# Kernel tuning notes

Measured on AMD Instinct MI355X. Metric: run time of the kernel, lower is better.

## Reference

```python
import jax, jax.numpy as jnp
import numpy as np
from jax import lax

B, T, D, H = 2, 2048, 512, 8
HD = D // H
EPS = 1e-5


def _layernorm(x, g, b):
    m = jnp.mean(x, axis=-1, keepdims=True)
    v = jnp.var(x, axis=-1, keepdims=True)
    return (x - m) / jnp.sqrt(v + EPS) * g + b


def setup_inputs() -> dict:
    key = jax.random.key(0)
    ks = jax.random.split(key, 16)
    s = 0.02
    return {
        "x": jax.random.normal(ks[0], (B, T, D), jnp.float32),
        "pe": jax.random.normal(ks[1], (B, T, D), jnp.float32),
        "conv_w": jax.random.normal(ks[2], (D, D, 3), jnp.float32) * s,   # OIH
        "conv_b": jnp.zeros((D,), jnp.float32),
        "in_proj_w": jax.random.normal(ks[3], (3 * D, D), jnp.float32) * s,
        "in_proj_b": jnp.zeros((3 * D,), jnp.float32),
        "out_proj_w": jax.random.normal(ks[4], (D, D), jnp.float32) * s,
        "out_proj_b": jnp.zeros((D,), jnp.float32),
        "ln1_g": jnp.ones((D,), jnp.float32),
        "ln1_b": jnp.zeros((D,), jnp.float32),
        "w1": jax.random.normal(ks[5], (2 * D, D), jnp.float32) * s,
        "b1": jnp.zeros((2 * D,), jnp.float32),
        "w2": jax.random.normal(ks[6], (D, 2 * D), jnp.float32) * s,
        "b2": jnp.zeros((D,), jnp.float32),
        "ln2_g": jnp.ones((D,), jnp.float32),
        "ln2_b": jnp.zeros((D,), jnp.float32),
    }


def reference(x, pe, conv_w, conv_b, in_proj_w, in_proj_b, out_proj_w,
              out_proj_b, ln1_g, ln1_b, w1, b1, w2, b2, ln2_g, ln2_b):
    Bv, Tv, Dv = x.shape
    window = max(Tv // 4, 1)
    half = window // 2
    idx = jnp.arange(Tv)
    blocked = jnp.abs(idx[:, None] - idx[None, :]) > half  # [T, T]
    mask = jnp.where(blocked, -jnp.inf, 0.0).astype(x.dtype)

    # Conv1d on values: x [B,T,D] -> [B,D,T], kernel3 pad1, back to [B,T,D]
    xT = jnp.transpose(x, (0, 2, 1))
    v_in = lax.conv_general_dilated(xT, conv_w, window_strides=(1,),
                                    padding=((1, 1),),
                                    dimension_numbers=("NCH", "OIH", "NCH"))
    v_in = jnp.transpose(v_in + conv_b[None, :, None], (0, 2, 1))

    # MultiheadAttention(q=x, k=x, v=v_in)
    Wq, Wk, Wv = jnp.split(in_proj_w, 3, axis=0)
    bq, bk, bv = jnp.split(in_proj_b, 3, axis=0)
    q = (x @ Wq.T + bq).reshape(Bv, Tv, H, HD).transpose(0, 2, 1, 3)
    k = (x @ Wk.T + bk).reshape(Bv, Tv, H, HD).transpose(0, 2, 1, 3)
    v = (v_in @ Wv.T + bv).reshape(Bv, Tv, H, HD).transpose(0, 2, 1, 3)

    scores = jnp.einsum("bhqd,bhkd->bhqk", q, k) / np.sqrt(HD).astype(x.dtype)
    scores = scores + mask[None, None]
    attn = jax.nn.softmax(scores, axis=-1)
    ctx = jnp.einsum("bhqk,bhkd->bhqd", attn, v)
    ctx = ctx.transpose(0, 2, 1, 3).reshape(Bv, Tv, Dv)
    attn_out = ctx @ out_proj_w.T + out_proj_b

    h = _layernorm(x + attn_out, ln1_g, ln1_b)
    ffn = jax.nn.relu(h @ w1.T + b1) @ w2.T + b2
    return _layernorm(h + ffn, ln2_g, ln2_b)
```

## Files before the change

### kernel.cpp

```cpp
#include <hip/hip_runtime.h>
#include <cstdint>
#include <cstddef>

static constexpr int kT  = 2048;
static constexpr int kD  = 512;
static constexpr int kB  = 2;
static constexpr int kN  = kB * kT;

using short8 = __attribute__((ext_vector_type(8))) short;
using f32x4  = __attribute__((ext_vector_type(4))) float;
typedef unsigned short ushort;

__device__ inline ushort f2bf(float f) {
  uint32_t u = __builtin_bit_cast(uint32_t, f);
  uint32_t r = (u + 0x7FFFu + ((u >> 16) & 1u)) >> 16;
  return (ushort)r;
}

#define GLOAD_LDS16(g, l)                                         \
  __builtin_amdgcn_global_load_lds(                               \
      (const __attribute__((address_space(1))) void*)(g),         \
      (__attribute__((address_space(3))) void*)(l), 16, 0, 0)

__global__ __launch_bounds__(256) void prep_kernel(
    const float* __restrict__ x,   const float* __restrict__ ipw,
    const float* __restrict__ opw, const float* __restrict__ w1,
    const float* __restrict__ w2,  const float* __restrict__ cw,
    ushort* __restrict__ xb,   ushort* __restrict__ ipwb,
    ushort* __restrict__ opwb, ushort* __restrict__ w1b,
    ushort* __restrict__ w2b,  ushort* __restrict__ wcat,
    ushort* __restrict__ acat)
{
  constexpr int C0 = 524288;
  constexpr int C1 = C0 + 196608;
  constexpr int C2 = C1 + 65536;
  constexpr int C3 = C2 + 131072;
  constexpr int C4 = C3 + 131072;
  constexpr int C5 = C4 + 262144;
  constexpr int C6 = C5 + 786432;

  auto cast4 = [](const float* in, ushort* out, int u) {
    float4 v = *reinterpret_cast<const float4*>(&in[(size_t)u * 4]);
    ushort o[4] = {f2bf(v.x), f2bf(v.y), f2bf(v.z), f2bf(v.w)};
    *reinterpret_cast<uint2*>(&out[(size_t)u * 4]) =
        *reinterpret_cast<uint2*>(o);
  };

  for (int u = blockIdx.x * 256 + threadIdx.x; u < C6; u += gridDim.x * 256) {
    if (u < C0) {
      cast4(x, xb, u);
    } else if (u < C1) {
      cast4(ipw, ipwb, u - C0);
    } else if (u < C2) {
      cast4(opw, opwb, u - C1);
    } else if (u < C3) {
      cast4(w1, w1b, u - C2);
    } else if (u < C4) {
      cast4(w2, w2b, u - C3);
    } else if (u < C5) {
      int t = u - C4;
      int o = t >> 9, i = t & 511;
      const float* src = &cw[(size_t)(o * kD + i) * 3];
      ushort* dst = &wcat[(size_t)o * (3 * kD) + i];
#pragma unroll
      for (int tap = 0; tap < 3; ++tap) dst[tap * kD] = f2bf(src[tap]);
    } else {
      int t = u - C5;
      int m = t / 192, r = t - m * 192;
      int tap = r >> 6, i8 = r & 63;
      int tib = (m & (kT - 1)) + tap - 1;
      ushort ob[8] = {0, 0, 0, 0, 0, 0, 0, 0};
      if (tib >= 0 && tib < kT) {
        const float* src = &x[(size_t)(m + tap - 1) * kD + i8 * 8];
        float4 v0 = *reinterpret_cast<const float4*>(src);
        float4 v1 = *reinterpret_cast<const float4*>(src + 4);
        ob[0] = f2bf(v0.x); ob[1] = f2bf(v0.y); ob[2] = f2bf(v0.z);
        ob[3] = f2bf(v0.w); ob[4] = f2bf(v1.x); ob[5] = f2bf(v1.y);
        ob[6] = f2bf(v1.z); ob[7] = f2bf(v1.w);
      }
      *reinterpret_cast<uint4*>(
          &acat[(size_t)m * (3 * kD) + tap * kD + i8 * 8]) =
          *reinterpret_cast<uint4*>(ob);
    }
  }
}

template <typename OutT, int RELU>
__global__ __launch_bounds__(256) void gemm_bf16(
    const ushort* __restrict__ A, const ushort* __restrict__ W,
    const float* __restrict__ bias, OutT* __restrict__ C,
    int M, int Nn, int K)
{
  __shared__ __align__(16) ushort As[3][64 * 64];
  __shared__ __align__(16) ushort Bs[3][64 * 64];
  const int tid = threadIdx.x;
  const int lane = tid & 63, w = tid >> 6;
  const int wr = w >> 1, wc = w & 1;
  const int m0 = blockIdx.x * 64, n0 = blockIdx.y * 64;
  const int fr = lane & 15, g = lane >> 4;

  f32x4 acc[2][2];
#pragma unroll
  for (int i = 0; i < 2; ++i)
#pragma unroll
    for (int j = 0; j < 2; ++j) acc[i][j] = {0.f, 0.f, 0.f, 0.f};

  const int u0 = tid, u1 = tid + 256;
  const int r0s = u0 >> 3, c0s = (u0 & 7) ^ (r0s & 7);
  const int r1s = u1 >> 3, c1s = (u1 & 7) ^ (r1s & 7);
  const ushort* gA0 = A + (size_t)(m0 + r0s) * K + c0s * 8;
  const ushort* gA1 = A + (size_t)(m0 + r1s) * K + c1s * 8;
  const ushort* gB0 = W + (size_t)(n0 + r0s) * K + c0s * 8;
  const ushort* gB1 = W + (size_t)(n0 + r1s) * K + c1s * 8;
  const int ld0 = w * 512;
  const int ld1 = 2048 + w * 512;

  auto stage = [&](int buf, int k0) {
    GLOAD_LDS16(gA0 + k0, &As[buf][ld0]);
    GLOAD_LDS16(gA1 + k0, &As[buf][ld1]);
    GLOAD_LDS16(gB0 + k0, &Bs[buf][ld0]);
    GLOAD_LDS16(gB1 + k0, &Bs[buf][ld1]);
  };

  const int nt = K >> 6;
  stage(0, 0);
  stage(1, 64);
  int cur = 0, b2 = 2;
  for (int t = 0; t < nt; ++t) {
    if (t + 2 < nt) {
      stage(b2, (t + 2) << 6);
      asm volatile("s_waitcnt vmcnt(8)" ::: "memory");
    } else if (t + 1 < nt) {
      asm volatile("s_waitcnt vmcnt(4)" ::: "memory");
    } else {
      asm volatile("s_waitcnt vmcnt(0)" ::: "memory");
    }
    __builtin_amdgcn_s_barrier();
    __builtin_amdgcn_sched_barrier(0);

    short8 a[2][2], b[2][2];
#pragma unroll
    for (int m = 0; m < 2; ++m)
#pragma unroll
      for (int kc = 0; kc < 2; ++kc) {
        int r = wr * 32 + m * 16 + fr;
        a[m][kc] = *reinterpret_cast<const short8*>(
            &As[cur][r * 64 + (((kc * 4 + g) ^ (r & 7)) * 8)]);
      }
#pragma unroll
    for (int n = 0; n < 2; ++n)
#pragma unroll
      for (int kc = 0; kc < 2; ++kc) {
        int r = wc * 32 + n * 16 + fr;
        b[n][kc] = *reinterpret_cast<const short8*>(
            &Bs[cur][r * 64 + (((kc * 4 + g) ^ (r & 7)) * 8)]);
      }
#pragma unroll
    for (int m = 0; m < 2; ++m)
#pragma unroll
      for (int n = 0; n < 2; ++n)
#pragma unroll
        for (int kc = 0; kc < 2; ++kc)
          acc[m][n] = __builtin_amdgcn_mfma_f32_16x16x32_bf16(
              a[m][kc], b[n][kc], acc[m][n], 0, 0, 0);

    __builtin_amdgcn_sched_barrier(0);
    __builtin_amdgcn_s_barrier();
    cur = cur == 2 ? 0 : cur + 1;
    b2 = b2 == 2 ? 0 : b2 + 1;
  }

  float bv[2];
#pragma unroll
  for (int n = 0; n < 2; ++n) bv[n] = bias[n0 + wc * 32 + n * 16 + fr];
#pragma unroll
  for (int m = 0; m < 2; ++m) {
#pragma unroll
    for (int j = 0; j < 4; ++j) {
      int row = m0 + wr * 32 + m * 16 + g * 4 + j;
#pragma unroll
      for (int n = 0; n < 2; ++n) {
        int col = n0 + wc * 32 + n * 16 + fr;
        float v = acc[m][n][j] + bv[n];
        if (RELU) v = fmaxf(v, 0.f);
        if constexpr (sizeof(OutT) == 2)
          C[(size_t)row * Nn + col] = (OutT)f2bf(v);
        else
          C[(size_t)row * Nn + col] = (OutT)v;
      }
    }
  }
}

__global__ __launch_bounds__(256) void attn_mfma(
    const ushort* __restrict__ QK, const ushort* __restrict__ V,
    ushort* __restrict__ Ctx)
{
  constexpr int PAD = 72;
  __shared__ __align__(16) ushort Ks[64 * 64];
  __shared__ __align__(16) ushort Vt[64][PAD];
  __shared__ __align__(16) ushort Pl[4][16][PAD];
  const int tid = threadIdx.x;
  const int lane = tid & 63, w = tid >> 6;
  const int l15 = lane & 15, g = lane >> 4;
  const int bh = blockIdx.y;
  const int b = bh >> 3, h = bh & 7;
  const int r0 = blockIdx.x * 64;
  const int rowbase = b * kT;
  const int qrow0 = r0 + w * 16;
  const int t_lo = max(r0 - 256, 0);
  const int t_last = min(r0 + 256, kT - 64);
  const int ntiles = ((t_last - t_lo) >> 6) + 1;

  short8 qf[2];
  {
    const size_t qb = (size_t)(rowbase + qrow0 + l15) * 1024 + h * 64 + g * 8;
    qf[0] = *reinterpret_cast<const short8*>(&QK[qb]);
    qf[1] = *reinterpret_cast<const short8*>(&QK[qb + 32]);
  }

  f32x4 acc[4];
#pragma unroll
  for (int d = 0; d < 4; ++d) acc[d] = {0.f, 0.f, 0.f, 0.f};
  float mrun[4] = {-1e30f, -1e30f, -1e30f, -1e30f};
  float lrun[4] = {0.f, 0.f, 0.f, 0.f};

  for (int tt = 0; tt < ntiles; ++tt) {
    const int j0 = t_lo + tt * 64;

#pragma unroll
    for (int c = 0; c < 2; ++c) {
      int u = c * 256 + tid;
      int row = u >> 3;
      int col8 = (u & 7) ^ (row & 7);
      const ushort* src =
          &QK[(size_t)(rowbase + j0 + row) * 1024 + 512 + h * 64 + col8 * 8];
      GLOAD_LDS16(src, &Ks[(c * 256 + w * 64) * 8]);
    }
#pragma unroll
    for (int i = 0; i < 2; ++i) {
      int dg = w + 4 * i;
      uint4 vv = *reinterpret_cast<const uint4*>(
          &V[(size_t)(rowbase + j0 + lane) * 512 + h * 64 + dg * 8]);
      ushort tmp[8];
      *reinterpret_cast<uint4*>(tmp) = vv;
#pragma unroll
      for (int e = 0; e < 8; ++e) Vt[dg * 8 + e][lane] = tmp[e];
    }
    __syncthreads();

    f32x4 s[4];
#pragma unroll
    for (int n = 0; n < 4; ++n) {
      f32x4 z = {0.f, 0.f, 0.f, 0.f};
#pragma unroll
      for (int kc = 0; kc < 2; ++kc) {
        int row = n * 16 + l15;
        int unit = row * 8 + ((kc * 4 + g) ^ (row & 7));
        short8 kb = *reinterpret_cast<const short8*>(&Ks[unit * 8]);
        z = __builtin_amdgcn_mfma_f32_16x16x32_bf16(qf[kc], kb, z, 0, 0, 0);
      }
      s[n] = z;
    }
#pragma unroll
    for (int n = 0; n < 4; ++n)
#pragma unroll
      for (int j = 0; j < 4; ++j) {
        int col = j0 + n * 16 + l15;
        int qr = qrow0 + g * 4 + j;
        int dlt = col - qr;
        float v = s[n][j] * 0.125f;
        s[n][j] = (dlt > 256 || dlt < -256) ? -1e30f : v;
      }
    float pn[4][4];
    float sold[4];
#pragma unroll
    for (int j = 0; j < 4; ++j) {
      float mx = fmaxf(fmaxf(s[0][j], s[1][j]), fmaxf(s[2][j], s[3][j]));
      mx = fmaxf(mx, __shfl_xor(mx, 1));
      mx = fmaxf(mx, __shfl_xor(mx, 2));
      mx = fmaxf(mx, __shfl_xor(mx, 4));
      mx = fmaxf(mx, __shfl_xor(mx, 8));
      float mnew = fmaxf(mrun[j], mx);
      float sc = __expf(mrun[j] - mnew);
      mrun[j] = mnew;
      sold[j] = sc;
      float rs = 0.f;
#pragma unroll
      for (int n = 0; n < 4; ++n) {
        float p = __expf(s[n][j] - mnew);
        pn[n][j] = p;
        rs += p;
      }
      rs += __shfl_xor(rs, 1);
      rs += __shfl_xor(rs, 2);
      rs += __shfl_xor(rs, 4);
      rs += __shfl_xor(rs, 8);
      lrun[j] = lrun[j] * sc + rs;
    }
#pragma unroll
    for (int d = 0; d < 4; ++d)
#pragma unroll
      for (int j = 0; j < 4; ++j) acc[d][j] *= sold[j];
#pragma unroll
    for (int n = 0; n < 4; ++n)
#pragma unroll
      for (int j = 0; j < 4; ++j)
        Pl[w][g * 4 + j][n * 16 + l15] = f2bf(pn[n][j]);
    asm volatile("s_waitcnt lgkmcnt(0)" ::: "memory");
    __builtin_amdgcn_sched_barrier(0);

    short8 pa[2];
    pa[0] = *reinterpret_cast<const short8*>(&Pl[w][l15][g * 8]);
    pa[1] = *reinterpret_cast<const short8*>(&Pl[w][l15][32 + g * 8]);
#pragma unroll
    for (int d = 0; d < 4; ++d) {
#pragma unroll
      for (int kc = 0; kc < 2; ++kc) {
        short8 vb = *reinterpret_cast<const short8*>(
            &Vt[d * 16 + l15][kc * 32 + g * 8]);
        acc[d] = __builtin_amdgcn_mfma_f32_16x16x32_bf16(pa[kc], vb, acc[d], 0, 0, 0);
      }
    }
    __syncthreads();
  }

  float inv[4];
#pragma unroll
  for (int j = 0; j < 4; ++j) inv[j] = 1.f / lrun[j];
#pragma unroll
  for (int d = 0; d < 4; ++d)
#pragma unroll
    for (int j = 0; j < 4; ++j) {
      float v = acc[d][j] * inv[j];
      Ctx[(size_t)(rowbase + qrow0 + g * 4 + j) * 512 + h * 64 + d * 16 + l15] =
          f2bf(v);
    }
}

__global__ __launch_bounds__(256) void ln_kernel(
    const float* __restrict__ A, const float* __restrict__ Bq,
    const float* __restrict__ G, const float* __restrict__ Bt,
    float* __restrict__ Out, ushort* __restrict__ OutB)
{
  const int lane = threadIdx.x & 63;
  const int wv = threadIdx.x >> 6;
  const int row = blockIdx.x * 4 + wv;
  const size_t base = (size_t)row * kD + lane * 8;

  float4 a0 = *reinterpret_cast<const float4*>(&A[base]);
  float4 a1 = *reinterpret_cast<const float4*>(&A[base + 4]);
  float4 b0 = *reinterpret_cast<const float4*>(&Bq[base]);
  float4 b1 = *reinterpret_cast<const float4*>(&Bq[base + 4]);
  float x[8] = {a0.x + b0.x, a0.y + b0.y, a0.z + b0.z, a0.w + b0.w,
                a1.x + b1.x, a1.y + b1.y, a1.z + b1.z, a1.w + b1.w};
  float s = 0.f, ss = 0.f;
#pragma unroll
  for (int i = 0; i < 8; ++i) { s += x[i]; ss += x[i] * x[i]; }
#pragma unroll
  for (int o = 1; o < 64; o <<= 1) {
    s += __shfl_xor(s, o, 64);
    ss += __shfl_xor(ss, o, 64);
  }
  const float mean = s * (1.f / kD);
  const float var = ss * (1.f / kD) - mean * mean;
  const float rs = rsqrtf(var + 1e-5f);

  const int c = lane * 8;
  float4 g0 = *reinterpret_cast<const float4*>(&G[c]);
  float4 g1 = *reinterpret_cast<const float4*>(&G[c + 4]);
  float4 t0 = *reinterpret_cast<const float4*>(&Bt[c]);
  float4 t1 = *reinterpret_cast<const float4*>(&Bt[c + 4]);
  float y[8];
  y[0] = (x[0] - mean) * rs * g0.x + t0.x;
  y[1] = (x[1] - mean) * rs * g0.y + t0.y;
  y[2] = (x[2] - mean) * rs * g0.z + t0.z;
  y[3] = (x[3] - mean) * rs * g0.w + t0.w;
  y[4] = (x[4] - mean) * rs * g1.x + t1.x;
  y[5] = (x[5] - mean) * rs * g1.y + t1.y;
  y[6] = (x[6] - mean) * rs * g1.z + t1.z;
  y[7] = (x[7] - mean) * rs * g1.w + t1.w;
  *reinterpret_cast<float4*>(&Out[base]) = {y[0], y[1], y[2], y[3]};
  *reinterpret_cast<float4*>(&Out[base + 4]) = {y[4], y[5], y[6], y[7]};
  if (OutB) {
    ushort ob[8];
#pragma unroll
    for (int i = 0; i < 8; ++i) ob[i] = f2bf(y[i]);
    *reinterpret_cast<uint4*>(&OutB[base]) = *reinterpret_cast<uint4*>(ob);
  }
}

extern "C" void kernel_launch(void* const* d_in, const int* in_sizes, int n_in,
                              void* d_out, int out_size, void* d_ws, size_t ws_size,
                              hipStream_t stream)
{
  const float* x   = (const float*)d_in[0];
  const float* cw  = (const float*)d_in[2];
  const float* cb  = (const float*)d_in[3];
  const float* ipw = (const float*)d_in[4];
  const float* ipb = (const float*)d_in[5];
  const float* opw = (const float*)d_in[6];
  const float* opb = (const float*)d_in[7];
  const float* g1  = (const float*)d_in[8];
  const float* b1n = (const float*)d_in[9];
  const float* w1  = (const float*)d_in[10];
  const float* bb1 = (const float*)d_in[11];
  const float* w2  = (const float*)d_in[12];
  const float* bb2 = (const float*)d_in[13];
  const float* g2  = (const float*)d_in[14];
  const float* b2n = (const float*)d_in[15];
  float* out = (float*)d_out;

  char* p = (char*)d_ws;
  auto take = [&](size_t bytes) {
    char* q = p; p += (bytes + 255) & ~size_t(255); return q;
  };
  ushort* xb    = (ushort*)take((size_t)kN * kD * 2);
  char*  acat_r =          take((size_t)kN * 3 * kD * 2);
  ushort* acat  = (ushort*)acat_r;
  ushort* wcat  = (ushort*)take((size_t)kD * 3 * kD * 2);
  ushort* ipwb  = (ushort*)take((size_t)3 * kD * kD * 2);
  ushort* opwb  = (ushort*)take((size_t)kD * kD * 2);
  ushort* w1b   = (ushort*)take((size_t)2 * kD * kD * 2);
  ushort* w2b   = (ushort*)take((size_t)2 * kD * kD * 2);
  ushort* convo = (ushort*)take((size_t)kN * kD * 2);
  char*  qk_r   =          take((size_t)kN * 2 * kD * 2);
  ushort* qkb   = (ushort*)qk_r;
  ushort* vbb   = (ushort*)take((size_t)kN * kD * 2);
  ushort* ctx   = (ushort*)take((size_t)kN * kD * 2);
  float* hbuf   = (float*)take((size_t)kN * kD * 4);
  ushort* hb    = (ushort*)take((size_t)kN * kD * 2);
  float* attno  = (float*)acat_r;
  ushort* f1    = (ushort*)qk_r;
  float* f2     = (float*)acat_r;

  dim3 blk(256);
  prep_kernel<<<dim3(2048), blk, 0, stream>>>(
      x, ipw, opw, w1, w2, cw, xb, ipwb, opwb, w1b, w2b, wcat, acat);

  gemm_bf16<ushort, 0><<<dim3(kN / 64, kD / 64), blk, 0, stream>>>(
      acat, wcat, cb, convo, kN, kD, 3 * kD);
  gemm_bf16<ushort, 0><<<dim3(kN / 64, 1024 / 64), blk, 0, stream>>>(
      xb, ipwb, ipb, qkb, kN, 1024, kD);
  gemm_bf16<ushort, 0><<<dim3(kN / 64, kD / 64), blk, 0, stream>>>(
      convo, ipwb + (size_t)1024 * kD, ipb + 1024, vbb, kN, kD, kD);
  attn_mfma<<<dim3(kT / 64, kB * 8), blk, 0, stream>>>(qkb, vbb, ctx);
  gemm_bf16<float, 0><<<dim3(kN / 64, kD / 64), blk, 0, stream>>>(
      ctx, opwb, opb, attno, kN, kD, kD);
  ln_kernel<<<dim3(kN / 4), blk, 0, stream>>>(x, attno, g1, b1n, hbuf, hb);
  gemm_bf16<ushort, 1><<<dim3(kN / 64, 1024 / 64), blk, 0, stream>>>(
      hb, w1b, bb1, f1, kN, 1024, kD);
  gemm_bf16<float, 0><<<dim3(kN / 64, kD / 64), blk, 0, stream>>>(
      f1, w2b, bb2, f2, kN, kD, 2 * kD);
  ln_kernel<<<dim3(kN / 4), blk, 0, stream>>>(hbuf, f2, g2, b2n, out, nullptr);
}
```

Before: 210.9 us.

## Use BK=128 double buffering in GEMM and prefetch K/V tiles in attention

The GEMM switches from a triple-buffered 64-wide K tile to a double-buffered 128-wide K tile, with 8 async LDS loads per stage and 16 MFMAs per barrier pair. This halves the number of barriers and gives more MFMA work per synchronisation. The attention kernel now double-buffers K and V in shared memory: it issues the next tile's K (async LDS) and V (into registers) before computing the current tile, then transposes V into the other buffer at the end of the iteration. This hides global load latency, at the cost of more LDS and registers, which may reduce occupancy.

```diff
diff --git a/kernel.cpp b/kernel.cpp
--- a/kernel.cpp
+++ b/kernel.cpp
@@ -91,8 +91,8 @@
     const float* __restrict__ bias, OutT* __restrict__ C,
     int M, int Nn, int K)
 {
-  __shared__ __align__(16) ushort As[3][64 * 64];
-  __shared__ __align__(16) ushort Bs[3][64 * 64];
+  __shared__ __align__(16) ushort As[2][64 * 128];
+  __shared__ __align__(16) ushort Bs[2][64 * 128];
   const int tid = threadIdx.x;
   const int lane = tid & 63, w = tid >> 6;
   const int wr = w >> 1, wc = w & 1;
@@ -105,69 +105,66 @@
 #pragma unroll
     for (int j = 0; j < 2; ++j) acc[i][j] = {0.f, 0.f, 0.f, 0.f};
 
-  const int u0 = tid, u1 = tid + 256;
-  const int r0s = u0 >> 3, c0s = (u0 & 7) ^ (r0s & 7);
-  const int r1s = u1 >> 3, c1s = (u1 & 7) ^ (r1s & 7);
-  const ushort* gA0 = A + (size_t)(m0 + r0s) * K + c0s * 8;
-  const ushort* gA1 = A + (size_t)(m0 + r1s) * K + c1s * 8;
-  const ushort* gB0 = W + (size_t)(n0 + r0s) * K + c0s * 8;
-  const ushort* gB1 = W + (size_t)(n0 + r1s) * K + c1s * 8;
-  const int ld0 = w * 512;
-  const int ld1 = 2048 + w * 512;
+  const ushort* gA[4];
+  const ushort* gB[4];
+#pragma unroll
+  for (int i = 0; i < 4; ++i) {
+    int u = i * 256 + tid;
+    int row = u >> 4, c = (u & 15) ^ (row & 7);
+    gA[i] = A + (size_t)(m0 + row) * K + c * 8;
+    gB[i] = W + (size_t)(n0 + row) * K + c * 8;
+  }
 
   auto stage = [&](int buf, int k0) {
-    GLOAD_LDS16(gA0 + k0, &As[buf][ld0]);
-    GLOAD_LDS16(gA1 + k0, &As[buf][ld1]);
-    GLOAD_LDS16(gB0 + k0, &Bs[buf][ld0]);
-    GLOAD_LDS16(gB1 + k0, &Bs[buf][ld1]);
-  };
-
-  const int nt = K >> 6;
+#pragma unroll
+    for (int i = 0; i < 4; ++i)
+      GLOAD_LDS16(gA[i] + k0, &As[buf][(i * 256 + w * 64) * 8]);
+#pragma unroll
+    for (int i = 0; i < 4; ++i)
+      GLOAD_LDS16(gB[i] + k0, &Bs[buf][(i * 256 + w * 64) * 8]);
+  };
+
+  const int nt = K >> 7;
   stage(0, 0);
-  stage(1, 64);
-  int cur = 0, b2 = 2;
   for (int t = 0; t < nt; ++t) {
-    if (t + 2 < nt) {
-      stage(b2, (t + 2) << 6);
+    const int buf = t & 1;
+    if (t + 1 < nt) {
+      stage(buf ^ 1, (t + 1) << 7);
       asm volatile("s_waitcnt vmcnt(8)" ::: "memory");
-    } else if (t + 1 < nt) {
-      asm volatile("s_waitcnt vmcnt(4)" ::: "memory");
     } else {
       asm volatile("s_waitcnt vmcnt(0)" ::: "memory");
     }
     __builtin_amdgcn_s_barrier();
     __builtin_amdgcn_sched_barrier(0);
 
-    short8 a[2][2], b[2][2];
+    short8 a[2][4], b[2][4];
 #pragma unroll
     for (int m = 0; m < 2; ++m)
 #pragma unroll
-      for (int kc = 0; kc < 2; ++kc) {
+      for (int kc = 0; kc < 4; ++kc) {
         int r = wr * 32 + m * 16 + fr;
         a[m][kc] = *reinterpret_cast<const short8*>(
-            &As[cur][r * 64 + (((kc * 4 + g) ^ (r & 7)) * 8)]);
+            &As[buf][(r * 16 + ((kc * 4 + g) ^ (r & 7))) * 8]);
       }
 #pragma unroll
     for (int n = 0; n < 2; ++n)
 #pragma unroll
-      for (int kc = 0; kc < 2; ++kc) {
+      for (int kc = 0; kc < 4; ++kc) {
         int r = wc * 32 + n * 16 + fr;
         b[n][kc] = *reinterpret_cast<const short8*>(
-            &Bs[cur][r * 64 + (((kc * 4 + g) ^ (r & 7)) * 8)]);
+            &Bs[buf][(r * 16 + ((kc * 4 + g) ^ (r & 7))) * 8]);
       }
 #pragma unroll
     for (int m = 0; m < 2; ++m)
 #pragma unroll
       for (int n = 0; n < 2; ++n)
 #pragma unroll
-        for (int kc = 0; kc < 2; ++kc)
+        for (int kc = 0; kc < 4; ++kc)
           acc[m][n] = __builtin_amdgcn_mfma_f32_16x16x32_bf16(
               a[m][kc], b[n][kc], acc[m][n], 0, 0, 0);
 
     __builtin_amdgcn_sched_barrier(0);
     __builtin_amdgcn_s_barrier();
-    cur = cur == 2 ? 0 : cur + 1;
-    b2 = b2 == 2 ? 0 : b2 + 1;
   }
 
   float bv[2];
@@ -197,8 +194,8 @@
     ushort* __restrict__ Ctx)
 {
   constexpr int PAD = 72;
-  __shared__ __align__(16) ushort Ks[64 * 64];
-  __shared__ __align__(16) ushort Vt[64][PAD];
+  __shared__ __align__(16) ushort Ks[2][64 * 64];
+  __shared__ __align__(16) ushort Vt[2][64][PAD];
   __shared__ __align__(16) ushort Pl[4][16][PAD];
   const int tid = threadIdx.x;
   const int lane = tid & 63, w = tid >> 6;
@@ -219,15 +216,8 @@
     qf[1] = *reinterpret_cast<const short8*>(&QK[qb + 32]);
   }
 
-  f32x4 acc[4];
-#pragma unroll
-  for (int d = 0; d < 4; ++d) acc[d] = {0.f, 0.f, 0.f, 0.f};
-  float mrun[4] = {-1e30f, -1e30f, -1e30f, -1e30f};
-  float lrun[4] = {0.f, 0.f, 0.f, 0.f};
-
-  for (int tt = 0; tt < ntiles; ++tt) {
-    const int j0 = t_lo + tt * 64;
-
+  uint4 vreg[2];
+  auto issueK = [&](int buf, int j0) {
 #pragma unroll
     for (int c = 0; c < 2; ++c) {
       int u = c * 256 + tid;
@@ -235,19 +225,45 @@
       int col8 = (u & 7) ^ (row & 7);
       const ushort* src =
           &QK[(size_t)(rowbase + j0 + row) * 1024 + 512 + h * 64 + col8 * 8];
-      GLOAD_LDS16(src, &Ks[(c * 256 + w * 64) * 8]);
-    }
+      GLOAD_LDS16(src, &Ks[buf][(c * 256 + w * 64) * 8]);
+    }
+  };
+  auto issueV = [&](int j0) {
+#pragma unroll
+    for (int i = 0; i < 2; ++i)
+      vreg[i] = *reinterpret_cast<const uint4*>(
+          &V[(size_t)(rowbase + j0 + lane) * 512 + h * 64 + (w + 4 * i) * 8]);
+  };
+  auto writeV = [&](int buf) {
 #pragma unroll
     for (int i = 0; i < 2; ++i) {
       int dg = w + 4 * i;
-      uint4 vv = *reinterpret_cast<const uint4*>(
-          &V[(size_t)(rowbase + j0 + lane) * 512 + h * 64 + dg * 8]);
       ushort tmp[8];
-      *reinterpret_cast<uint4*>(tmp) = vv;
-#pragma unroll
-      for (int e = 0; e < 8; ++e) Vt[dg * 8 + e][lane] = tmp[e];
-    }
-    __syncthreads();
+      *reinterpret_cast<uint4*>(tmp) = vreg[i];
+#pragma unroll
+      for (int e = 0; e < 8; ++e) Vt[buf][dg * 8 + e][lane] = tmp[e];
+    }
+  };
+
+  f32x4 acc[4];
+#pragma unroll
+  for (int d = 0; d < 4; ++d) acc[d] = {0.f, 0.f, 0.f, 0.f};
+  float mrun[4] = {-1e30f, -1e30f, -1e30f, -1e30f};
+  float lrun[4] = {0.f, 0.f, 0.f, 0.f};
+
+  issueK(0, t_lo);
+  issueV(t_lo);
+  asm volatile("s_waitcnt vmcnt(0)" ::: "memory");
+  writeV(0);
+  __syncthreads();
+
+  for (int tt = 0; tt < ntiles; ++tt) {
+    const int buf = tt & 1;
+    const int j0 = t_lo + tt * 64;
+    if (tt + 1 < ntiles) {
+      issueK(buf ^ 1, j0 + 64);
+      issueV(j0 + 64);
+    }
 
     f32x4 s[4];
 #pragma unroll
@@ -257,7 +273,7 @@
       for (int kc = 0; kc < 2; ++kc) {
         int row = n * 16 + l15;
         int unit = row * 8 + ((kc * 4 + g) ^ (row & 7));
-        short8 kb = *reinterpret_cast<const short8*>(&Ks[unit * 8]);
+        short8 kb = *reinterpret_cast<const short8*>(&Ks[buf][unit * 8]);
         z = __builtin_amdgcn_mfma_f32_16x16x32_bf16(qf[kc], kb, z, 0, 0, 0);
       }
       s[n] = z;
@@ -318,9 +334,14 @@
 #pragma unroll
       for (int kc = 0; kc < 2; ++kc) {
         short8 vb = *reinterpret_cast<const short8*>(
-            &Vt[d * 16 + l15][kc * 32 + g * 8]);
+            &Vt[buf][d * 16 + l15][kc * 32 + g * 8]);
         acc[d] = __builtin_amdgcn_mfma_f32_16x16x32_bf16(pa[kc], vb, acc[d], 0, 0, 0);
       }
+    }
+
+    if (tt + 1 < ntiles) {
+      asm volatile("s_waitcnt vmcnt(0)" ::: "memory");
+      writeV(buf ^ 1);
     }
     __syncthreads();
   }
```

After: 204.5 us. 1.03x faster.

## Fuse all stages into one persistent kernel with software grid barriers

Applied to the files above, without the earlier changes.

Replaces the ten separate kernel launches with a single 512-block persistent kernel. Stages are separated by atomic-counter grid barriers, and each block takes fixed GEMM, attention or layernorm tiles per stage. The attention loop now double-buffers K and V tiles so the next tile's loads overlap the current compute, and f2 gets its own buffer instead of aliasing acat. This removes launch gaps and tail overhead, at the cost of spin-barrier latency, fixed block-to-work mapping, and a reliance on all 512 blocks being co-resident (deadlock risk otherwise).

```diff
diff --git a/kernel.cpp b/kernel.cpp
--- a/kernel.cpp
+++ b/kernel.cpp
@@ -6,6 +6,7 @@
 static constexpr int kD  = 512;
 static constexpr int kB  = 2;
 static constexpr int kN  = kB * kT;
+static constexpr int NB  = 512;
 
 using short8 = __attribute__((ext_vector_type(8))) short;
 using f32x4  = __attribute__((ext_vector_type(4))) float;
@@ -22,15 +23,41 @@
       (const __attribute__((address_space(1))) void*)(g),         \
       (__attribute__((address_space(3))) void*)(l), 16, 0, 0)
 
-__global__ __launch_bounds__(256) void prep_kernel(
-    const float* __restrict__ x,   const float* __restrict__ ipw,
-    const float* __restrict__ opw, const float* __restrict__ w1,
-    const float* __restrict__ w2,  const float* __restrict__ cw,
-    ushort* __restrict__ xb,   ushort* __restrict__ ipwb,
-    ushort* __restrict__ opwb, ushort* __restrict__ w1b,
-    ushort* __restrict__ w2b,  ushort* __restrict__ wcat,
-    ushort* __restrict__ acat)
-{
+struct __align__(16) SmemGemm {
+  ushort As[3][64 * 64];
+  ushort Bs[3][64 * 64];
+};
+struct __align__(16) SmemAttn {
+  ushort Ks[2][64 * 64];
+  ushort Vt[2][64][72];
+  ushort Pl[4][16][72];
+};
+union SmemAll { SmemGemm g; SmemAttn a; };
+
+struct Args {
+  const float *x, *cw, *cb, *ipw, *ipb, *opw, *opb;
+  const float *g1, *b1n, *w1, *bb1, *w2, *bb2, *g2, *b2n;
+  float *out;
+  ushort *xb, *acat, *wcat, *ipwb, *opwb, *w1b, *w2b;
+  ushort *convo, *qkb, *vbb, *ctx, *hb, *f1;
+  float *hbuf, *attno, *f2;
+  int *bar;
+};
+
+__device__ __forceinline__ void gridbar(int* cnt, int phase) {
+  __syncthreads();
+  if (threadIdx.x == 0) {
+    __builtin_amdgcn_fence(__ATOMIC_RELEASE, "agent");
+    __hip_atomic_fetch_add(cnt, 1, __ATOMIC_RELAXED, __HIP_MEMORY_SCOPE_AGENT);
+    const int want = phase * NB;
+    while (__hip_atomic_load(cnt, __ATOMIC_RELAXED, __HIP_MEMORY_SCOPE_AGENT) < want)
+      __builtin_amdgcn_s_sleep(8);
+    __builtin_amdgcn_fence(__ATOMIC_ACQUIRE, "agent");
+  }
+  __syncthreads();
+}
+
+__device__ void prep_phase(const Args& a, int bid) {
   constexpr int C0 = 524288;
   constexpr int C1 = C0 + 196608;
   constexpr int C2 = C1 + 65536;
@@ -46,22 +73,22 @@
         *reinterpret_cast<uint2*>(o);
   };
 
-  for (int u = blockIdx.x * 256 + threadIdx.x; u < C6; u += gridDim.x * 256) {
+  for (int u = bid * 256 + threadIdx.x; u < C6; u += NB * 256) {
     if (u < C0) {
-      cast4(x, xb, u);
+      cast4(a.x, a.xb, u);
     } else if (u < C1) {
-      cast4(ipw, ipwb, u - C0);
+      cast4(a.ipw, a.ipwb, u - C0);
     } else if (u < C2) {
-      cast4(opw, opwb, u - C1);
+      cast4(a.opw, a.opwb, u - C1);
     } else if (u < C3) {
-      cast4(w1, w1b, u - C2);
+      cast4(a.w1, a.w1b, u - C2);
     } else if (u < C4) {
-      cast4(w2, w2b, u - C3);
+      cast4(a.w2, a.w2b, u - C3);
     } else if (u < C5) {
       int t = u - C4;
       int o = t >> 9, i = t & 511;
-      const float* src = &cw[(size_t)(o * kD + i) * 3];
-      ushort* dst = &wcat[(size_t)o * (3 * kD) + i];
+      const float* src = &a.cw[(size_t)(o * kD + i) * 3];
+      ushort* dst = &a.wcat[(size_t)o * (3 * kD) + i];
 #pragma unroll
       for (int tap = 0; tap < 3; ++tap) dst[tap * kD] = f2bf(src[tap]);
     } else {
@@ -71,7 +98,7 @@
       int tib = (m & (kT - 1)) + tap - 1;
       ushort ob[8] = {0, 0, 0, 0, 0, 0, 0, 0};
       if (tib >= 0 && tib < kT) {
-        const float* src = &x[(size_t)(m + tap - 1) * kD + i8 * 8];
+        const float* src = &a.x[(size_t)(m + tap - 1) * kD + i8 * 8];
         float4 v0 = *reinterpret_cast<const float4*>(src);
         float4 v1 = *reinterpret_cast<const float4*>(src + 4);
         ob[0] = f2bf(v0.x); ob[1] = f2bf(v0.y); ob[2] = f2bf(v0.z);
@@ -79,25 +106,24 @@
         ob[6] = f2bf(v1.z); ob[7] = f2bf(v1.w);
       }
       *reinterpret_cast<uint4*>(
-          &acat[(size_t)m * (3 * kD) + tap * kD + i8 * 8]) =
+          &a.acat[(size_t)m * (3 * kD) + tap * kD + i8 * 8]) =
           *reinterpret_cast<uint4*>(ob);
     }
   }
 }
 
 template <typename OutT, int RELU>
-__global__ __launch_bounds__(256) void gemm_bf16(
+__device__ void gemm_tile(SmemGemm& S,
     const ushort* __restrict__ A, const ushort* __restrict__ W,
     const float* __restrict__ bias, OutT* __restrict__ C,
-    int M, int Nn, int K)
+    int Nn, int K, int m0, int n0)
 {
-  __shared__ __align__(16) ushort As[3][64 * 64];
-  __shared__ __align__(16) ushort Bs[3][64 * 64];
   const int tid = threadIdx.x;
   const int lane = tid & 63, w = tid >> 6;
   const int wr = w >> 1, wc = w & 1;
-  const int m0 = blockIdx.x * 64, n0 = blockIdx.y * 64;
   const int fr = lane & 15, g = lane >> 4;
+
+  __syncthreads();
 
   f32x4 acc[2][2];
 #pragma unroll
@@ -116,10 +142,10 @@
   const int ld1 = 2048 + w * 512;
 
   auto stage = [&](int buf, int k0) {
-    GLOAD_LDS16(gA0 + k0, &As[buf][ld0]);
-    GLOAD_LDS16(gA1 + k0, &As[buf][ld1]);
-    GLOAD_LDS16(gB0 + k0, &Bs[buf][ld0]);
-    GLOAD_LDS16(gB1 + k0, &Bs[buf][ld1]);
+    GLOAD_LDS16(gA0 + k0, &S.As[buf][ld0]);
+    GLOAD_LDS16(gA1 + k0, &S.As[buf][ld1]);
+    GLOAD_LDS16(gB0 + k0, &S.Bs[buf][ld0]);
+    GLOAD_LDS16(gB1 + k0, &S.Bs[buf][ld1]);
   };
 
   const int nt = K >> 6;
@@ -138,22 +164,22 @@
     __builtin_amdgcn_s_barrier();
     __builtin_amdgcn_sched_barrier(0);
 
-    short8 a[2][2], b[2][2];
+    short8 av[2][2], bv[2][2];
 #pragma unroll
     for (int m = 0; m < 2; ++m)
 #pragma unroll
       for (int kc = 0; kc < 2; ++kc) {
         int r = wr * 32 + m * 16 + fr;
-        a[m][kc] = *reinterpret_cast<const short8*>(
-            &As[cur][r * 64 + (((kc * 4 + g) ^ (r & 7)) * 8)]);
+        av[m][kc] = *reinterpret_cast<const short8*>(
+            &S.As[cur][r * 64 + (((kc * 4 + g) ^ (r & 7)) * 8)]);
       }
 #pragma unroll
     for (int n = 0; n < 2; ++n)
 #pragma unroll
       for (int kc = 0; kc < 2; ++kc) {
         int r = wc * 32 + n * 16 + fr;
-        b[n][kc] = *reinterpret_cast<const short8*>(
-            &Bs[cur][r * 64 + (((kc * 4 + g) ^ (r & 7)) * 8)]);
+        bv[n][kc] = *reinterpret_cast<const short8*>(
+            &S.Bs[cur][r * 64 + (((kc * 4 + g) ^ (r & 7)) * 8)]);
       }
 #pragma unroll
     for (int m = 0; m < 2; ++m)
@@ -162,7 +188,7 @@
 #pragma unroll
         for (int kc = 0; kc < 2; ++kc)
           acc[m][n] = __builtin_amdgcn_mfma_f32_16x16x32_bf16(
-              a[m][kc], b[n][kc], acc[m][n], 0, 0, 0);
+              av[m][kc], bv[n][kc], acc[m][n], 0, 0, 0);
 
     __builtin_amdgcn_sched_barrier(0);
     __builtin_amdgcn_s_barrier();
@@ -170,9 +196,9 @@
     b2 = b2 == 2 ? 0 : b2 + 1;
   }
 
-  float bv[2];
-#pragma unroll
-  for (int n = 0; n < 2; ++n) bv[n] = bias[n0 + wc * 32 + n * 16 + fr];
+  float bb[2];
+#pragma unroll
+  for (int n = 0; n < 2; ++n) bb[n] = bias[n0 + wc * 32 + n * 16 + fr];
 #pragma unroll
   for (int m = 0; m < 2; ++m) {
 #pragma unroll
@@ -181,7 +207,7 @@
 #pragma unroll
       for (int n = 0; n < 2; ++n) {
         int col = n0 + wc * 32 + n * 16 + fr;
-        float v = acc[m][n][j] + bv[n];
+        float v = acc[m][n][j] + bb[n];
         if (RELU) v = fmaxf(v, 0.f);
         if constexpr (sizeof(OutT) == 2)
           C[(size_t)row * Nn + col] = (OutT)f2bf(v);
@@ -192,25 +218,22 @@
   }
 }
 
-__global__ __launch_bounds__(256) void attn_mfma(
-    const ushort* __restrict__ QK, const ushort* __restrict__ V,
-    ushort* __restrict__ Ctx)
-{
-  constexpr int PAD = 72;
-  __shared__ __align__(16) ushort Ks[64 * 64];
-  __shared__ __align__(16) ushort Vt[64][PAD];
-  __shared__ __align__(16) ushort Pl[4][16][PAD];
+__device__ void attn_tile(SmemAttn& S, const Args& a, int bid) {
   const int tid = threadIdx.x;
   const int lane = tid & 63, w = tid >> 6;
   const int l15 = lane & 15, g = lane >> 4;
-  const int bh = blockIdx.y;
+  const int qt = bid & 31, bh = bid >> 5;
   const int b = bh >> 3, h = bh & 7;
-  const int r0 = blockIdx.x * 64;
+  const int r0 = qt * 64;
   const int rowbase = b * kT;
   const int qrow0 = r0 + w * 16;
   const int t_lo = max(r0 - 256, 0);
   const int t_last = min(r0 + 256, kT - 64);
   const int ntiles = ((t_last - t_lo) >> 6) + 1;
+  const ushort* QK = a.qkb;
+  const ushort* V = a.vbb;
+
+  __syncthreads();
 
   short8 qf[2];
   {
@@ -219,15 +242,8 @@
     qf[1] = *reinterpret_cast<const short8*>(&QK[qb + 32]);
   }
 
-  f32x4 acc[4];
-#pragma unroll
-  for (int d = 0; d < 4; ++d) acc[d] = {0.f, 0.f, 0.f, 0.f};
-  float mrun[4] = {-1e30f, -1e30f, -1e30f, -1e30f};
-  float lrun[4] = {0.f, 0.f, 0.f, 0.f};
-
-  for (int tt = 0; tt < ntiles; ++tt) {
-    const int j0 = t_lo + tt * 64;
-
+  uint4 vreg[2];
+  auto issueK = [&](int buf, int j0) {
 #pragma unroll
     for (int c = 0; c < 2; ++c) {
       int u = c * 256 + tid;
@@ -235,19 +251,45 @@
       int col8 = (u & 7) ^ (row & 7);
       const ushort* src =
           &QK[(size_t)(rowbase + j0 + row) * 1024 + 512 + h * 64 + col8 * 8];
-      GLOAD_LDS16(src, &Ks[(c * 256 + w * 64) * 8]);
-    }
+      GLOAD_LDS16(src, &S.Ks[buf][(c * 256 + w * 64) * 8]);
+    }
+  };
+  auto issueV = [&](int j0) {
+#pragma unroll
+    for (int i = 0; i < 2; ++i)
+      vreg[i] = *reinterpret_cast<const uint4*>(
+          &V[(size_t)(rowbase + j0 + lane) * 512 + h * 64 + (w + 4 * i) * 8]);
+  };
+  auto writeV = [&](int buf) {
 #pragma unroll
     for (int i = 0; i < 2; ++i) {
       int dg = w + 4 * i;
-      uint4 vv = *reinterpret_cast<const uint4*>(
-          &V[(size_t)(rowbase + j0 + lane) * 512 + h * 64 + dg * 8]);
       ushort tmp[8];
-      *reinterpret_cast<uint4*>(tmp) = vv;
-#pragma unroll
-      for (int e = 0; e < 8; ++e) Vt[dg * 8 + e][lane] = tmp[e];
-    }
-    __syncthreads();
+      *reinterpret_cast<uint4*>(tmp) = vreg[i];
+#pragma unroll
+      for (int e = 0; e < 8; ++e) S.Vt[buf][dg * 8 + e][lane] = tmp[e];
+    }
+  };
+
+  f32x4 acc[4];
+#pragma unroll
+  for (int d = 0; d < 4; ++d) acc[d] = {0.f, 0.f, 0.f, 0.f};
+  float mrun[4] = {-1e30f, -1e30f, -1e30f, -1e30f};
+  float lrun[4] = {0.f, 0.f, 0.f, 0.f};
+
+  issueK(0, t_lo);
+  issueV(t_lo);
+  asm volatile("s_waitcnt vmcnt(0)" ::: "memory");
+  writeV(0);
+  __syncthreads();
+
+  for (int tt = 0; tt < ntiles; ++tt) {
+    const int buf = tt & 1;
+    const int j0 = t_lo + tt * 64;
+    if (tt + 1 < ntiles) {
+      issueK(buf ^ 1, j0 + 64);
+      issueV(j0 + 64);
+    }
 
     f32x4 s[4];
 #pragma unroll
@@ -257,7 +299,7 @@
       for (int kc = 0; kc < 2; ++kc) {
         int row = n * 16 + l15;
         int unit = row * 8 + ((kc * 4 + g) ^ (row & 7));
-        short8 kb = *reinterpret_cast<const short8*>(&Ks[unit * 8]);
+        short8 kb = *reinterpret_cast<const short8*>(&S.Ks[buf][unit * 8]);
         z = __builtin_amdgcn_mfma_f32_16x16x32_bf16(qf[kc], kb, z, 0, 0, 0);
       }
       s[n] = z;
@@ -306,21 +348,26 @@
     for (int n = 0; n < 4; ++n)
 #pragma unroll
       for (int j = 0; j < 4; ++j)
-        Pl[w][g * 4 + j][n * 16 + l15] = f2bf(pn[n][j]);
+        S.Pl[w][g * 4 + j][n * 16 + l15] = f2bf(pn[n][j]);
     asm volatile("s_waitcnt lgkmcnt(0)" ::: "memory");
     __builtin_amdgcn_sched_barrier(0);
 
     short8 pa[2];
-    pa[0] = *reinterpret_cast<const short8*>(&Pl[w][l15][g * 8]);
-    pa[1] = *reinterpret_cast<const short8*>(&Pl[w][l15][32 + g * 8]);
+    pa[0] = *reinterpret_cast<const short8*>(&S.Pl[w][l15][g * 8]);
+    pa[1] = *reinterpret_cast<const short8*>(&S.Pl[w][l15][32 + g * 8]);
 #pragma unroll
     for (int d = 0; d < 4; ++d) {
 #pragma unroll
       for (int kc = 0; kc < 2; ++kc) {
         short8 vb = *reinterpret_cast<const short8*>(
-            &Vt[d * 16 + l15][kc * 32 + g * 8]);
+            &S.Vt[buf][d * 16 + l15][kc * 32 + g * 8]);
         acc[d] = __builtin_amdgcn_mfma_f32_16x16x32_bf16(pa[kc], vb, acc[d], 0, 0, 0);
       }
+    }
+
+    if (tt + 1 < ntiles) {
+      asm volatile("s_waitcnt vmcnt(0)" ::: "memory");
+      writeV(buf ^ 1);
     }
     __syncthreads();
   }
@@ -333,124 +380,158 @@
 #pragma unroll
     for (int j = 0; j < 4; ++j) {
       float v = acc[d][j] * inv[j];
-      Ctx[(size_t)(rowbase + qrow0 + g * 4 + j) * 512 + h * 64 + d * 16 + l15] =
+      a.ctx[(size_t)(rowbase + qrow0 + g * 4 + j) * 512 + h * 64 + d * 16 + l15] =
           f2bf(v);
     }
 }
 
-__global__ __launch_bounds__(256) void ln_kernel(
-    const float* __restrict__ A, const float* __restrict__ Bq,
-    const float* __restrict__ G, const float* __restrict__ Bt,
-    float* __restrict__ Out, ushort* __restrict__ OutB)
+__device__ void ln_rows(const float* __restrict__ A, const float* __restrict__ Bq,
+                        const float* __restrict__ G, const float* __restrict__ Bt,
+                        float* __restrict__ Out, ushort* __restrict__ OutB,
+                        int bid)
 {
   const int lane = threadIdx.x & 63;
   const int wv = threadIdx.x >> 6;
-  const int row = blockIdx.x * 4 + wv;
-  const size_t base = (size_t)row * kD + lane * 8;
-
-  float4 a0 = *reinterpret_cast<const float4*>(&A[base]);
-  float4 a1 = *reinterpret_cast<const float4*>(&A[base + 4]);
-  float4 b0 = *reinterpret_cast<const float4*>(&Bq[base]);
-  float4 b1 = *reinterpret_cast<const float4*>(&Bq[base + 4]);
-  float x[8] = {a0.x + b0.x, a0.y + b0.y, a0.z + b0.z, a0.w + b0.w,
-                a1.x + b1.x, a1.y + b1.y, a1.z + b1.z, a1.w + b1.w};
-  float s = 0.f, ss = 0.f;
-#pragma unroll
-  for (int i = 0; i < 8; ++i) { s += x[i]; ss += x[i] * x[i]; }
-#pragma unroll
-  for (int o = 1; o < 64; o <<= 1) {
-    s += __shfl_xor(s, o, 64);
-    ss += __shfl_xor(ss, o, 64);
-  }
-  const float mean = s * (1.f / kD);
-  const float var = ss * (1.f / kD) - mean * mean;
-  const float rs = rsqrtf(var + 1e-5f);
-
-  const int c = lane * 8;
-  float4 g0 = *reinterpret_cast<const float4*>(&G[c]);
-  float4 g1 = *reinterpret_cast<const float4*>(&G[c + 4]);
-  float4 t0 = *reinterpret_cast<const float4*>(&Bt[c]);
-  float4 t1 = *reinterpret_cast<const float4*>(&Bt[c + 4]);
-  float y[8];
-  y[0] = (x[0] - mean) * rs * g0.x + t0.x;
-  y[1] = (x[1] - mean) * rs * g0.y + t0.y;
-  y[2] = (x[2] - mean) * rs * g0.z + t0.z;
-  y[3] = (x[3] - mean) * rs * g0.w + t0.w;
-  y[4] = (x[4] - mean) * rs * g1.x + t1.x;
-  y[5] = (x[5] - mean) * rs * g1.y + t1.y;
-  y[6] = (x[6] - mean) * rs * g1.z + t1.z;
-  y[7] = (x[7] - mean) * rs * g1.w + t1.w;
-  *reinterpret_cast<float4*>(&Out[base]) = {y[0], y[1], y[2], y[3]};
-  *reinterpret_cast<float4*>(&Out[base + 4]) = {y[4], y[5], y[6], y[7]};
-  if (OutB) {
-    ushort ob[8];
-#pragma unroll
-    for (int i = 0; i < 8; ++i) ob[i] = f2bf(y[i]);
-    *reinterpret_cast<uint4*>(&OutB[base]) = *reinterpret_cast<uint4*>(ob);
-  }
+#pragma unroll
+  for (int rr = 0; rr < 2; ++rr) {
+    const int row = bid * 8 + wv * 2 + rr;
+    const size_t base = (size_t)row * kD + lane * 8;
+
+    float4 a0 = *reinterpret_cast<const float4*>(&A[base]);
+    float4 a1 = *reinterpret_cast<const float4*>(&A[base + 4]);
+    float4 b0 = *reinterpret_cast<const float4*>(&Bq[base]);
+    float4 b1 = *reinterpret_cast<const float4*>(&Bq[base + 4]);
+    float x[8] = {a0.x + b0.x, a0.y + b0.y, a0.z + b0.z, a0.w + b0.w,
+                  a1.x + b1.x, a1.y + b1.y, a1.z + b1.z, a1.w + b1.w};
+    float s = 0.f, ss = 0.f;
+#pragma unroll
+    for (int i = 0; i < 8; ++i) { s += x[i]; ss += x[i] * x[i]; }
+#pragma unroll
+    for (int o = 1; o < 64; o <<= 1) {
+      s += __shfl_xor(s, o, 64);
+      ss += __shfl_xor(ss, o, 64);
+    }
+    const float mean = s * (1.f / kD);
+    const float var = ss * (1.f / kD) - mean * mean;
+    const float rs = rsqrtf(var + 1e-5f);
+
+    const int c = lane * 8;
+    float4 g0 = *reinterpret_cast<const float4*>(&G[c]);
+    float4 g1 = *reinterpret_cast<const float4*>(&G[c + 4]);
+    float4 t0 = *reinterpret_cast<const float4*>(&Bt[c]);
+    float4 t1 = *reinterpret_cast<const float4*>(&Bt[c + 4]);
+    float y[8];
+    y[0] = (x[0] - mean) * rs * g0.x + t0.x;
+    y[1] = (x[1] - mean) * rs * g0.y + t0.y;
+    y[2] = (x[2] - mean) * rs * g0.z + t0.z;
+    y[3] = (x[3] - mean) * rs * g0.w + t0.w;
+    y[4] = (x[4] - mean) * rs * g1.x + t1.x;
+    y[5] = (x[5] - mean) * rs * g1.y + t1.y;
+    y[6] = (x[6] - mean) * rs * g1.z + t1.z;
+    y[7] = (x[7] - mean) * rs * g1.w + t1.w;
+    *reinterpret_cast<float4*>(&Out[base]) = {y[0], y[1], y[2], y[3]};
+    *reinterpret_cast<float4*>(&Out[base + 4]) = {y[4], y[5], y[6], y[7]};
+    if (OutB) {
+      ushort ob[8];
+#pragma unroll
+      for (int i = 0; i < 8; ++i) ob[i] = f2bf(y[i]);
+      *reinterpret_cast<uint4*>(&OutB[base]) = *reinterpret_cast<uint4*>(ob);
+    }
+  }
+}
+
+__global__ __launch_bounds__(256, 2) void mega_kernel(Args a) {
+  __shared__ SmemAll sm;
+  const int bid = blockIdx.x;
+
+  prep_phase(a, bid);
+  gridbar(a.bar, 1);
+
+  gemm_tile<ushort, 0>(sm.g, a.acat, a.wcat, a.cb, a.convo,
+                       kD, 3 * kD, (bid >> 3) * 64, (bid & 7) * 64);
+  {
+    int q0 = bid, q1 = bid + 512;
+    gemm_tile<ushort, 0>(sm.g, a.xb, a.ipwb, a.ipb, a.qkb,
+                         1024, kD, (q0 >> 4) * 64, (q0 & 15) * 64);
+    gemm_tile<ushort, 0>(sm.g, a.xb, a.ipwb, a.ipb, a.qkb,
+                         1024, kD, (q1 >> 4) * 64, (q1 & 15) * 64);
+  }
+  gridbar(a.bar, 2);
+
+  gemm_tile<ushort, 0>(sm.g, a.convo, a.ipwb + (size_t)1024 * kD,
+                       a.ipb + 1024, a.vbb, kD, kD,
+                       (bid >> 3) * 64, (bid & 7) * 64);
+  gridbar(a.bar, 3);
+
+  attn_tile(sm.a, a, bid);
+  gridbar(a.bar, 4);
+
+  gemm_tile<float, 0>(sm.g, a.ctx, a.opwb, a.opb, a.attno,
+                      kD, kD, (bid >> 3) * 64, (bid & 7) * 64);
+  gridbar(a.bar, 5);
+
+  ln_rows(a.x, a.attno, a.g1, a.b1n, a.hbuf, a.hb, bid);
+  gridbar(a.bar, 6);
+
+  gemm_tile<ushort, 1>(sm.g, a.hb, a.w1b, a.bb1, a.f1,
+                       1024, kD, (bid >> 4) * 64, (bid & 15) * 64);
+  gemm_tile<ushort, 1>(sm.g, a.hb, a.w1b, a.bb1, a.f1,
+                       1024, kD, ((bid + 512) >> 4) * 64, ((bid + 512) & 15) * 64);
+  gridbar(a.bar, 7);
+
+  gemm_tile<float, 0>(sm.g, a.f1, a.w2b, a.bb2, a.f2,
+                      kD, 2 * kD, (bid >> 3) * 64, (bid & 7) * 64);
+  gridbar(a.bar, 8);
+
+  ln_rows(a.hbuf, a.f2, a.g2, a.b2n, a.out, nullptr, bid);
 }
 
 extern "C" void kernel_launch(void* const* d_in, const int* in_sizes, int n_in,
                               void* d_out, int out_size, void* d_ws, size_t ws_size,
                               hipStream_t stream)
 {
-  const float* x   = (const float*)d_in[0];
-  const float* cw  = (const float*)d_in[2];
-  const float* cb  = (const float*)d_in[3];
-  const float* ipw = (const float*)d_in[4];
-  const float* ipb = (const float*)d_in[5];
-  const float* opw = (const float*)d_in[6];
-  const float* opb = (const float*)d_in[7];
-  const float* g1  = (const float*)d_in[8];
-  const float* b1n = (const float*)d_in[9];
-  const float* w1  = (const float*)d_in[10];
-  const float* bb1 = (const float*)d_in[11];
-  const float* w2  = (const float*)d_in[12];
-  const float* bb2 = (const float*)d_in[13];
-  const float* g2  = (const float*)d_in[14];
-  const float* b2n = (const float*)d_in[15];
-  float* out = (float*)d_out;
+  Args a;
+  a.x   = (const float*)d_in[0];
+  a.cw  = (const float*)d_in[2];
+  a.cb  = (const float*)d_in[3];
+  a.ipw = (const float*)d_in[4];
+  a.ipb = (const float*)d_in[5];
+  a.opw = (const float*)d_in[6];
+  a.opb = (const float*)d_in[7];
+  a.g1  = (const float*)d_in[8];
+  a.b1n = (const float*)d_in[9];
+  a.w1  = (const float*)d_in[10];
+  a.bb1 = (const float*)d_in[11];
+  a.w2  = (const float*)d_in[12];
+  a.bb2 = (const float*)d_in[13];
+  a.g2  = (const float*)d_in[14];
+  a.b2n = (const float*)d_in[15];
+  a.out = (float*)d_out;
 
   char* p = (char*)d_ws;
   auto take = [&](size_t bytes) {
     char* q = p; p += (bytes + 255) & ~size_t(255); return q;
   };
-  ushort* xb    = (ushort*)take((size_t)kN * kD * 2);
-  char*  acat_r =          take((size_t)kN * 3 * kD * 2);
-  ushort* acat  = (ushort*)acat_r;
-  ushort* wcat  = (ushort*)take((size_t)kD * 3 * kD * 2);
-  ushort* ipwb  = (ushort*)take((size_t)3 * kD * kD * 2);
-  ushort* opwb  = (ushort*)take((size_t)kD * kD * 2);
-  ushort* w1b   = (ushort*)take((size_t)2 * kD * kD * 2);
-  ushort* w2b   = (ushort*)take((size_t)2 * kD * kD * 2);
-  ushort* convo = (ushort*)take((size_t)kN * kD * 2);
-  char*  qk_r   =          take((size_t)kN * 2 * kD * 2);
-  ushort* qkb   = (ushort*)qk_r;
-  ushort* vbb   = (ushort*)take((size_t)kN * kD * 2);
-  ushort* ctx   = (ushort*)take((size_t)kN * kD * 2);
-  float* hbuf   = (float*)take((size_t)kN * kD * 4);
-  ushort* hb    = (ushort*)take((size_t)kN * kD * 2);
-  float* attno  = (float*)acat_r;
-  ushort* f1    = (ushort*)qk_r;
-  float* f2     = (float*)acat_r;
-
-  dim3 blk(256);
-  prep_kernel<<<dim3(2048), blk, 0, stream>>>(
-      x, ipw, opw, w1, w2, cw, xb, ipwb, opwb, w1b, w2b, wcat, acat);
-
-  gemm_bf16<ushort, 0><<<dim3(kN / 64, kD / 64), blk, 0, stream>>>(
-      acat, wcat, cb, convo, kN, kD, 3 * kD);
-  gemm_bf16<ushort, 0><<<dim3(kN / 64, 1024 / 64), blk, 0, stream>>>(
-      xb, ipwb, ipb, qkb, kN, 1024, kD);
-  gemm_bf16<ushort, 0><<<dim3(kN / 64, kD / 64), blk, 0, stream>>>(
-      convo, ipwb + (size_t)1024 * kD, ipb + 1024, vbb, kN, kD, kD);
-  attn_mfma<<<dim3(kT / 64, kB * 8), blk, 0, stream>>>(qkb, vbb, ctx);
-  gemm_bf16<float, 0><<<dim3(kN / 64, kD / 64), blk, 0, stream>>>(
-      ctx, opwb, opb, attno, kN, kD, kD);
-  ln_kernel<<<dim3(kN / 4), blk, 0, stream>>>(x, attno, g1, b1n, hbuf, hb);
-  gemm_bf16<ushort, 1><<<dim3(kN / 64, 1024 / 64), blk, 0, stream>>>(
-      hb, w1b, bb1, f1, kN, 1024, kD);
-  gemm_bf16<float, 0><<<dim3(kN / 64, kD / 64), blk, 0, stream>>>(
-      f1, w2b, bb2, f2, kN, kD, 2 * kD);
-  ln_kernel<<<dim3(kN / 4), blk, 0, stream>>>(hbuf, f2, g2, b2n, out, nullptr);
-}
+  a.bar  = (int*)take(256);
+  a.xb   = (ushort*)take((size_t)kN * kD * 2);
+  char* acat_r =      take((size_t)kN * 3 * kD * 2);
+  a.acat = (ushort*)acat_r;
+  a.wcat = (ushort*)take((size_t)kD * 3 * kD * 2);
+  a.ipwb = (ushort*)take((size_t)3 * kD * kD * 2);
+  a.opwb = (ushort*)take((size_t)kD * kD * 2);
+  a.w1b  = (ushort*)take((size_t)2 * kD * kD * 2);
+  a.w2b  = (ushort*)take((size_t)2 * kD * kD * 2);
+  a.convo= (ushort*)take((size_t)kN * kD * 2);
+  char* qk_r =        take((size_t)kN * 2 * kD * 2);
+  a.qkb  = (ushort*)qk_r;
+  a.vbb  = (ushort*)take((size_t)kN * kD * 2);
+  a.ctx  = (ushort*)take((size_t)kN * kD * 2);
+  a.hbuf = (float*)take((size_t)kN * kD * 4);
+  a.hb   = (ushort*)take((size_t)kN * kD * 2);
+  a.attno= (float*)acat_r;
+  a.f1   = (ushort*)qk_r;
+  a.f2   = (float*)take((size_t)kN * kD * 4);
+
+  (void)hipMemsetAsync(a.bar, 0, 256, stream);
+  mega_kernel<<<dim3(NB), dim3(256), 0, stream>>>(a);
+}
```

Measured after the change: 573.2 us. +171.8%, slower.
